# Performance work log

Hardware: AMD Instinct MI355X
Metric: run time of the kernel (lower is better)

## Reference

```python
import jax, jax.numpy as jnp
import numpy as np

N_NODES = 100000
N_EDGES = 1600000
F_IN = 128
HID = 64
HORIZON = 100
NUM_TARGETS = 3


def setup_inputs() -> dict:
    key = jax.random.key(0)
    ks = jax.random.split(key, 7)
    x = jax.random.normal(ks[0], (N_NODES, F_IN), dtype=jnp.float32)
    edge_index = jax.random.randint(ks[1], (2, N_EDGES), 0, N_NODES, dtype=jnp.int64)
    s = 1.0 / np.sqrt(F_IN)
    W_l = jax.random.uniform(ks[2], (HID, F_IN), jnp.float32, -s, s)
    b_l = jax.random.uniform(ks[3], (HID,), jnp.float32, -s, s)
    W_r = jax.random.uniform(ks[4], (HID, F_IN), jnp.float32, -s, s)
    s2 = 1.0 / np.sqrt(HID)
    W_out = jax.random.uniform(ks[5], (NUM_TARGETS * HORIZON, HID), jnp.float32, -s2, s2)
    b_out = jax.random.uniform(ks[6], (NUM_TARGETS * HORIZON,), jnp.float32, -s2, s2)
    return {"x": x, "edge_index": edge_index, "W_l": W_l, "b_l": b_l,
            "W_r": W_r, "W_out": W_out, "b_out": b_out}


def reference(x, edge_index, W_l, b_l, W_r, W_out, b_out):
    n = x.shape[0]
    src, dst = edge_index[0], edge_index[1]
    # gather neighbor features and mean-aggregate per destination node
    msgs = x[src]  # [E, F_IN]
    agg = jax.ops.segment_sum(msgs, dst, num_segments=n)  # [N, F_IN]
    cnt = jax.ops.segment_sum(jnp.ones((edge_index.shape[1],), x.dtype), dst, num_segments=n)
    mean = agg / jnp.maximum(cnt, 1.0)[:, None]
    # SAGEConv: lin_l(aggregated) + lin_r(root), bias only on lin_l
    h = jnp.einsum('nf,hf->nh', mean, W_l) + b_l + jnp.einsum('nf,hf->nh', x, W_r)
    h = jax.nn.relu(h)
    out = jnp.einsum('nh,oh->no', h, W_out) + b_out  # [N, NUM_TARGETS*HORIZON]
    return out.reshape(-1, HORIZON)
```

## Files before the change

kernel.cpp:

```cpp
#include <hip/hip_runtime.h>

#define N_NODES 100000
#define F_IN 128
#define HID 64
#define OUT_F 300
#define WO_ROWS 320
#define NBKT 782
#define BCAP 16
#define ECAP 2688
#define PART_BLOCKS 512
#define GEMM_BLOCKS 391

typedef short bf8 __attribute__((ext_vector_type(8)));
typedef float f32x4 __attribute__((ext_vector_type(4)));

__device__ inline unsigned short f2bf(float f) {
    unsigned u = __builtin_bit_cast(unsigned, f);
    u += 0x7fff + ((u >> 16) & 1);
    return (unsigned short)(u >> 16);
}
__device__ inline float b2f(unsigned short h) {
    return __builtin_bit_cast(float, (unsigned)h << 16);
}

__global__ void k_prep(const float* __restrict__ Wl, const float* __restrict__ Wr,
                       const float* __restrict__ Wout,
                       unsigned short* __restrict__ Wc, unsigned short* __restrict__ Wo,
                       int* __restrict__ gcur) {
    int idx = blockIdx.x * blockDim.x + threadIdx.x;
    if (idx < 128 * 128) {
        int c = idx >> 7, k = idx & 127;
        float v = (c < HID) ? Wl[c * F_IN + k] : Wr[(c - HID) * F_IN + k];
        Wc[idx] = f2bf(v);
    } else if (idx < 128 * 128 + WO_ROWS * HID) {
        int j = idx - 128 * 128;
        int o = j >> 6, k = j & 63;
        Wo[j] = (o < OUT_F) ? f2bf(Wout[o * HID + k]) : (unsigned short)0;
    } else {
        int b = idx - 128 * 128 - WO_ROWS * HID;
        if (b < NBKT) gcur[b] = 0;
    }
}

__global__ __launch_bounds__(256) void k_pg(const int* __restrict__ ei,
                                            int* __restrict__ gcur,
                                            unsigned* __restrict__ pedges, int nE,
                                            const float* __restrict__ x,
                                            const unsigned short* __restrict__ Wc,
                                            unsigned short* __restrict__ yz) {
    if (blockIdx.x < PART_BLOCKS) {
        __shared__ unsigned buf[NBKT][BCAP];
        __shared__ int bcnt[NBKT];
        __shared__ unsigned rpk[256];
        __shared__ int rbk[256];
        __shared__ int rcnt;
        const int tid = threadIdx.x;
        for (int i = tid; i < NBKT; i += 256) bcnt[i] = 0;
        if (tid == 0) rcnt = 0;
        __syncthreads();
        const int per = (nE + PART_BLOCKS - 1) / PART_BLOCKS;
        const int e0 = blockIdx.x * per;
        const int e1 = min(e0 + per, nE);
        for (int base = e0; base < e1; base += 256) {
            const int e = base + tid;
            if (e < e1) {
                int src = ei[e];
                int dst = ei[nE + e];
                int b = dst >> 7;
                unsigned pk = ((unsigned)src << 7) | (unsigned)(dst & 127);
                int pos = atomicAdd(&bcnt[b], 1);
                if (pos < BCAP) buf[b][pos] = pk;
                else { int r = atomicAdd(&rcnt, 1); rpk[r] = pk; rbk[r] = b; }
            }
            __syncthreads();
            while (true) {
                for (int bb = tid; bb < NBKT; bb += 256) {
                    if (bcnt[bb] >= BCAP) {
                        int gp = atomicAdd(&gcur[bb], BCAP);
                        unsigned* dst = pedges + (size_t)bb * ECAP + gp;
#pragma unroll
                        for (int i = 0; i < BCAP; ++i) dst[i] = buf[bb][i];
                        bcnt[bb] = 0;
                    }
                }
                __syncthreads();
                int nr = rcnt;
                unsigned mpk = 0; int mb = -1;
                if (tid < nr) { mpk = rpk[tid]; mb = rbk[tid]; }
                __syncthreads();
                if (nr == 0) break;
                if (tid == 0) rcnt = 0;
                __syncthreads();
                if (mb >= 0) {
                    int pos = atomicAdd(&bcnt[mb], 1);
                    if (pos < BCAP) buf[mb][pos] = mpk;
                    else { int r = atomicAdd(&rcnt, 1); rpk[r] = mpk; rbk[r] = mb; }
                }
                __syncthreads();
            }
        }
        for (int bb = tid; bb < NBKT; bb += 256) {
            int c = bcnt[bb];
            if (c > 0) {
                int gp = atomicAdd(&gcur[bb], c);
                unsigned* dst = pedges + (size_t)bb * ECAP + gp;
                for (int i = 0; i < c; ++i) dst[i] = buf[bb][i];
            }
        }
    } else {
        const int wv = threadIdx.x >> 6;
        const int nb = (blockIdx.x - PART_BLOCKS) * 256 + wv * 64;
        if (nb >= N_NODES) return;
        const int lane = threadIdx.x & 63;
        const int lm = lane & 15, lk = lane >> 4;

        f32x4 acc[4][8];
#pragma unroll
        for (int a = 0; a < 4; ++a)
#pragma unroll
            for (int b = 0; b < 8; ++b) acc[a][b] = f32x4{0.f, 0.f, 0.f, 0.f};

#pragma unroll
        for (int kt = 0; kt < 4; ++kt) {
            const int ko = kt * 32 + lk * 8;
            bf8 af[4], bw[8];
#pragma unroll
            for (int mt = 0; mt < 4; ++mt) {
                int row = nb + mt * 16 + lm;
                if (row >= N_NODES) row = N_NODES - 1;
                const float* xp = x + (size_t)row * F_IN + ko;
                float4 v0 = *(const float4*)xp;
                float4 v1 = *(const float4*)(xp + 4);
                bf8 t;
                t[0] = (short)f2bf(v0.x); t[1] = (short)f2bf(v0.y);
                t[2] = (short)f2bf(v0.z); t[3] = (short)f2bf(v0.w);
                t[4] = (short)f2bf(v1.x); t[5] = (short)f2bf(v1.y);
                t[6] = (short)f2bf(v1.z); t[7] = (short)f2bf(v1.w);
                af[mt] = t;
            }
#pragma unroll
            for (int nt = 0; nt < 8; ++nt)
                bw[nt] = *reinterpret_cast<const bf8*>(Wc + (nt * 16 + lm) * 128 + ko);
#pragma unroll
            for (int mt = 0; mt < 4; ++mt)
#pragma unroll
                for (int nt = 0; nt < 8; ++nt)
                    acc[mt][nt] = __builtin_amdgcn_mfma_f32_16x16x32_bf16(af[mt], bw[nt], acc[mt][nt], 0, 0, 0);
        }
#pragma unroll
        for (int mt = 0; mt < 4; ++mt)
#pragma unroll
            for (int r = 0; r < 4; ++r) {
                int node = nb + mt * 16 + lk * 4 + r;
                if (node < N_NODES) {
#pragma unroll
                    for (int nt = 0; nt < 8; ++nt)
                        yz[(size_t)node * 128 + nt * 16 + lm] = f2bf(acc[mt][nt][r]);
                }
            }
    }
}

__global__ __launch_bounds__(512) void k_agg3(const unsigned short* __restrict__ yz,
                                              const unsigned* __restrict__ pedges,
                                              const int* __restrict__ gcur,
                                              const float* __restrict__ bl,
                                              unsigned short* __restrict__ h) {
    __shared__ unsigned esrc[ECAP];
    __shared__ int hcnt[128], hoff[128], hcur[128];
    const int tid = threadIdx.x, lane = tid & 63, wv = tid >> 6;
    const int bkt = blockIdx.x;
    int cnt = gcur[bkt]; if (cnt > ECAP) cnt = ECAP;
    const size_t base = (size_t)bkt * ECAP;
    if (tid < 128) hcnt[tid] = 0;
    __syncthreads();
    for (int i = tid; i < cnt; i += 512)
        atomicAdd(&hcnt[pedges[base + i] & 127], 1);
    __syncthreads();
    if (tid < 64) {
        int a = hcnt[2 * tid], b = hcnt[2 * tid + 1];
        int s = a + b;
#pragma unroll
        for (int d = 1; d < 64; d <<= 1) { int t = __shfl_up(s, d, 64); if (lane >= d) s += t; }
        int ex = s - (a + b);
        hoff[2 * tid] = ex;     hcur[2 * tid] = ex;
        hoff[2 * tid + 1] = ex + a; hcur[2 * tid + 1] = ex + a;
    }
    __syncthreads();
    for (int i = tid; i < cnt; i += 512) {
        unsigned e = pedges[base + i];
        int p = atomicAdd(&hcur[e & 127], 1);
        esrc[p] = e >> 7;
    }
    __syncthreads();
    const int q = lane >> 4;
    const int f4 = (lane & 15) * 4;
    float4 blv = *(const float4*)(bl + f4);
    for (int loc = wv; loc < 128; loc += 8) {
        int node = bkt * 128 + loc;
        if (node >= N_NODES) break;
        int st = hoff[loc], dg = hcnt[loc];
        float s0 = 0.f, s1 = 0.f, s2 = 0.f, s3 = 0.f;
        int j = 0;
        for (; j + 8 <= dg; j += 8) {
            unsigned eA = esrc[st + j + q];
            unsigned eB = esrc[st + j + 4 + q];
            uint2 uA = *(const uint2*)(yz + (size_t)eA * 128 + f4);
            uint2 uB = *(const uint2*)(yz + (size_t)eB * 128 + f4);
            s0 += b2f(uA.x & 0xffff) + b2f(uB.x & 0xffff);
            s1 += b2f(uA.x >> 16)    + b2f(uB.x >> 16);
            s2 += b2f(uA.y & 0xffff) + b2f(uB.y & 0xffff);
            s3 += b2f(uA.y >> 16)    + b2f(uB.y >> 16);
        }
        if (j + 4 <= dg) {
            unsigned eA = esrc[st + j + q];
            uint2 uA = *(const uint2*)(yz + (size_t)eA * 128 + f4);
            s0 += b2f(uA.x & 0xffff);
            s1 += b2f(uA.x >> 16);
            s2 += b2f(uA.y & 0xffff);
            s3 += b2f(uA.y >> 16);
            j += 4;
        }
        int rem = dg - j;
        if (q < rem) {
            unsigned eA = esrc[st + j + q];
            uint2 uA = *(const uint2*)(yz + (size_t)eA * 128 + f4);
            s0 += b2f(uA.x & 0xffff);
            s1 += b2f(uA.x >> 16);
            s2 += b2f(uA.y & 0xffff);
            s3 += b2f(uA.y >> 16);
        }
        s0 += __shfl_xor(s0, 16); s0 += __shfl_xor(s0, 32);
        s1 += __shfl_xor(s1, 16); s1 += __shfl_xor(s1, 32);
        s2 += __shfl_xor(s2, 16); s2 += __shfl_xor(s2, 32);
        s3 += __shfl_xor(s3, 16); s3 += __shfl_xor(s3, 32);
        if (q == 0) {
            float inv = 1.0f / fmaxf((float)dg, 1.0f);
            uint2 zu = *(const uint2*)(yz + (size_t)node * 128 + HID + f4);
            float v0 = s0 * inv + b2f(zu.x & 0xffff) + blv.x;
            float v1 = s1 * inv + b2f(zu.x >> 16)    + blv.y;
            float v2 = s2 * inv + b2f(zu.y & 0xffff) + blv.z;
            float v3 = s3 * inv + b2f(zu.y >> 16)    + blv.w;
            uint2 hv;
            hv.x = (unsigned)f2bf(fmaxf(v0, 0.f)) | ((unsigned)f2bf(fmaxf(v1, 0.f)) << 16);
            hv.y = (unsigned)f2bf(fmaxf(v2, 0.f)) | ((unsigned)f2bf(fmaxf(v3, 0.f)) << 16);
            *(uint2*)(h + (size_t)node * HID + f4) = hv;
        }
    }
}

__global__ __launch_bounds__(256, 2) void k_fused2(
    const unsigned short* __restrict__ h, const unsigned short* __restrict__ Wo,
    const float* __restrict__ bout, float* __restrict__ out) {

    __shared__ float sout[64 * OUT_F];
    const int tid = threadIdx.x;
    const int lane = tid & 63;
    const int mt = tid >> 6;
    const int nb = blockIdx.x * 64;
    const int lm = lane & 15, lk = lane >> 4;

    int row = nb + mt * 16 + lm;
    if (row >= N_NODES) row = N_NODES - 1;
    bf8 ah[2];
#pragma unroll
    for (int k2 = 0; k2 < 2; ++k2)
        ah[k2] = *reinterpret_cast<const bf8*>(h + (size_t)row * HID + k2 * 32 + lk * 8);

    for (int g = 0; g < 5; ++g) {
        f32x4 acc2[4];
#pragma unroll
        for (int b = 0; b < 4; ++b) acc2[b] = f32x4{0.f, 0.f, 0.f, 0.f};
#pragma unroll
        for (int k2 = 0; k2 < 2; ++k2) {
            bf8 bw[4];
#pragma unroll
            for (int nt = 0; nt < 4; ++nt)
                bw[nt] = *reinterpret_cast<const bf8*>(
                    Wo + (size_t)((g * 4 + nt) * 16 + lm) * HID + k2 * 32 + lk * 8);
#pragma unroll
            for (int nt = 0; nt < 4; ++nt)
                acc2[nt] = __builtin_amdgcn_mfma_f32_16x16x32_bf16(ah[k2], bw[nt], acc2[nt], 0, 0, 0);
        }
#pragma unroll
        for (int nt = 0; nt < 4; ++nt) {
            int o = g * 64 + nt * 16 + lm;
            if (o < OUT_F) {
                float bo = bout[o];
#pragma unroll
                for (int r = 0; r < 4; ++r) {
                    int locn = mt * 16 + lk * 4 + r;
                    sout[locn * OUT_F + o] = acc2[nt][r] + bo;
                }
            }
        }
    }
    __syncthreads();
    const int nvalid = min(64, N_NODES - nb);
    const int total = nvalid * OUT_F;
    float* op = out + (size_t)nb * OUT_F;
    for (int i = tid; i < total; i += 256) op[i] = sout[i];
}

extern "C" void kernel_launch(void* const* d_in, const int* in_sizes, int n_in,
                              void* d_out, int out_size, void* d_ws, size_t ws_size,
                              hipStream_t stream) {
    const float* x    = (const float*)d_in[0];
    const int*   ei   = (const int*)d_in[1];
    const float* Wl   = (const float*)d_in[2];
    const float* bl   = (const float*)d_in[3];
    const float* Wr   = (const float*)d_in[4];
    const float* Wout = (const float*)d_in[5];
    const float* bout = (const float*)d_in[6];
    float* out = (float*)d_out;

    int nE = in_sizes[1] / 2;

    unsigned short* yz = (unsigned short*)d_ws;
    unsigned short* h  = yz + (size_t)N_NODES * 128;
    unsigned* pedges = (unsigned*)(h + (size_t)N_NODES * HID);
    int* gcur  = (int*)(pedges + (size_t)NBKT * ECAP);
    unsigned short* Wc = (unsigned short*)(gcur + NBKT);
    unsigned short* Wo = Wc + 128 * 128;

    int prep_n = 128 * 128 + WO_ROWS * HID + NBKT;
    k_prep<<<(prep_n + 255) / 256, 256, 0, stream>>>(Wl, Wr, Wout, Wc, Wo, gcur);
    k_pg<<<PART_BLOCKS + GEMM_BLOCKS, 256, 0, stream>>>(ei, gcur, pedges, nE, x, Wc, yz);
    k_agg3<<<NBKT, 512, 0, stream>>>(yz, pedges, gcur, bl, h);
    k_fused2<<<(N_NODES + 63) / 64, 256, 0, stream>>>(h, Wo, bout, out);
}
```

Before: 154.3 us.

## Replace overflow-retry bucket buffers with per-chunk counting sort in partition

```diff
diff --git a/kernel.cpp b/kernel.cpp
--- a/kernel.cpp
+++ b/kernel.cpp
@@ -6,10 +6,10 @@
 #define OUT_F 300
 #define WO_ROWS 320
 #define NBKT 782
-#define BCAP 16
 #define ECAP 2688
-#define PART_BLOCKS 512
+#define PART_BLOCKS 256
 #define GEMM_BLOCKS 391
+#define SORT_CAP 6400
 
 typedef short bf8 __attribute__((ext_vector_type(8)));
 typedef float f32x4 __attribute__((ext_vector_type(4)));
@@ -49,63 +49,55 @@
                                             const unsigned short* __restrict__ Wc,
                                             unsigned short* __restrict__ yz) {
     if (blockIdx.x < PART_BLOCKS) {
-        __shared__ unsigned buf[NBKT][BCAP];
-        __shared__ int bcnt[NBKT];
-        __shared__ unsigned rpk[256];
-        __shared__ int rbk[256];
-        __shared__ int rcnt;
-        const int tid = threadIdx.x;
-        for (int i = tid; i < NBKT; i += 256) bcnt[i] = 0;
-        if (tid == 0) rcnt = 0;
-        __syncthreads();
+        __shared__ unsigned sorted[SORT_CAP];
+        __shared__ int hcnt[1024], hoff[1024], hcur[1024];
+        __shared__ int wpre[8];
+        const int tid = threadIdx.x, lane = tid & 63, wid = tid >> 6;
         const int per = (nE + PART_BLOCKS - 1) / PART_BLOCKS;
         const int e0 = blockIdx.x * per;
         const int e1 = min(e0 + per, nE);
-        for (int base = e0; base < e1; base += 256) {
-            const int e = base + tid;
-            if (e < e1) {
-                int src = ei[e];
-                int dst = ei[nE + e];
-                int b = dst >> 7;
+        for (int cb = e0; cb < e1; cb += SORT_CAP) {
+            const int cnt = min(SORT_CAP, e1 - cb);
+#pragma unroll
+            for (int i = 0; i < 4; ++i) hcnt[tid * 4 + i] = 0;
+            __syncthreads();
+            for (int i = tid; i < cnt; i += 256)
+                atomicAdd(&hcnt[ei[nE + cb + i] >> 7], 1);
+            __syncthreads();
+            int c0 = hcnt[tid * 4], c1 = hcnt[tid * 4 + 1];
+            int c2 = hcnt[tid * 4 + 2], c3 = hcnt[tid * 4 + 3];
+            int tsum = c0 + c1 + c2 + c3;
+            int s = tsum;
+#pragma unroll
+            for (int d = 1; d < 64; d <<= 1) { int t = __shfl_up(s, d, 64); if (lane >= d) s += t; }
+            if (lane == 63) wpre[wid] = s;
+            __syncthreads();
+            if (tid == 0) { int run = 0; for (int w = 0; w < 4; ++w) { int t = wpre[w]; wpre[w] = run; run += t; } }
+            __syncthreads();
+            int excl = wpre[wid] + (s - tsum);
+            hoff[tid * 4 + 0] = excl;                 hcur[tid * 4 + 0] = excl;
+            hoff[tid * 4 + 1] = excl + c0;            hcur[tid * 4 + 1] = excl + c0;
+            hoff[tid * 4 + 2] = excl + c0 + c1;       hcur[tid * 4 + 2] = excl + c0 + c1;
+            hoff[tid * 4 + 3] = excl + c0 + c1 + c2;  hcur[tid * 4 + 3] = excl + c0 + c1 + c2;
+            __syncthreads();
+            for (int i = tid; i < cnt; i += 256) {
+                int src = ei[cb + i];
+                int dst = ei[nE + cb + i];
                 unsigned pk = ((unsigned)src << 7) | (unsigned)(dst & 127);
-                int pos = atomicAdd(&bcnt[b], 1);
-                if (pos < BCAP) buf[b][pos] = pk;
-                else { int r = atomicAdd(&rcnt, 1); rpk[r] = pk; rbk[r] = b; }
-            }
-            __syncthreads();
-            while (true) {
-                for (int bb = tid; bb < NBKT; bb += 256) {
-                    if (bcnt[bb] >= BCAP) {
-                        int gp = atomicAdd(&gcur[bb], BCAP);
-                        unsigned* dst = pedges + (size_t)bb * ECAP + gp;
-#pragma unroll
-                        for (int i = 0; i < BCAP; ++i) dst[i] = buf[bb][i];
-                        bcnt[bb] = 0;
-                    }
+                int p = atomicAdd(&hcur[dst >> 7], 1);
+                sorted[p] = pk;
+            }
+            __syncthreads();
+            for (int b = tid; b < NBKT; b += 256) {
+                int c = hcnt[b];
+                if (c > 0) {
+                    int gp = atomicAdd(&gcur[b], c);
+                    unsigned* dst = pedges + (size_t)b * ECAP + gp;
+                    int off = hoff[b];
+                    for (int i = 0; i < c; ++i) dst[i] = sorted[off + i];
                 }
-                __syncthreads();
-                int nr = rcnt;
-                unsigned mpk = 0; int mb = -1;
-                if (tid < nr) { mpk = rpk[tid]; mb = rbk[tid]; }
-                __syncthreads();
-                if (nr == 0) break;
-                if (tid == 0) rcnt = 0;
-                __syncthreads();
-                if (mb >= 0) {
-                    int pos = atomicAdd(&bcnt[mb], 1);
-                    if (pos < BCAP) buf[mb][pos] = mpk;
-                    else { int r = atomicAdd(&rcnt, 1); rpk[r] = mpk; rbk[r] = mb; }
-                }
-                __syncthreads();
-            }
-        }
-        for (int bb = tid; bb < NBKT; bb += 256) {
-            int c = bcnt[bb];
-            if (c > 0) {
-                int gp = atomicAdd(&gcur[bb], c);
-                unsigned* dst = pedges + (size_t)bb * ECAP + gp;
-                for (int i = 0; i < c; ++i) dst[i] = buf[bb][i];
-            }
+            }
+            __syncthreads();
         }
     } else {
         const int wv = threadIdx.x >> 6;
```

Measured after the change: 142.0 us. -8.0%, faster.
